# Performance work log

Hardware: AMD Instinct MI355X
Metric: run time of the kernel (lower is better)

## Reference

```python
import jax, jax.numpy as jnp
import numpy as np

PI = 3.14159265359  # TFPI constant from the source


def expected_relu(mu, sigma_sq):
    # Expected ReLU of N(mu, sigma_sq); exact ReLU where sigma_sq == 0 (observed).
    missing = sigma_sq != 0.0
    imputed = jnp.where(missing, sigma_sq, 1e-20)
    s = jnp.sqrt(imputed)
    w = mu / s
    vals = s * (jnp.exp(-0.5 * w * w) / jnp.sqrt(2.0 * PI)
                + 0.5 * w * (1.0 + jax.scipy.special.erf(w / jnp.sqrt(2.0))))
    return jnp.where(missing, vals, 0.5 * (mu + jnp.abs(mu)))


def setup_inputs() -> dict:
    key = jax.random.key(0)
    k0, k1, k2, k3, k4 = jax.random.split(key, 5)
    N, P, C, U = 65536, 256, 3, 512
    x = jax.random.normal(k0, (N, P), dtype=jnp.float32)
    nan_mask = jax.random.bernoulli(k1, 0.15, (N, P))
    x = jnp.where(nan_mask, jnp.nan, x)
    component_means = 0.5 * jax.random.normal(k2, (P, C), dtype=jnp.float32)
    component_vars = jax.random.uniform(k3, (P, C), dtype=jnp.float32, minval=0.5, maxval=1.5)
    component_logits = jnp.ones((C,), dtype=jnp.float32)
    kernel = jax.random.normal(k4, (P, U), dtype=jnp.float32) / np.float32(np.sqrt(P))
    bias = jnp.zeros((U,), dtype=jnp.float32)
    return {"x": x, "component_means": component_means, "component_vars": component_vars,
            "component_logits": component_logits, "kernel": kernel, "bias": bias}


def reference(x, component_means, component_vars, component_logits, kernel, bias):
    # x: [N, P] with NaNs; component_means/vars: [P, C]; logits: [C]; kernel: [P, U]; bias: [U]
    nan_mask = jnp.isnan(x)                       # [N, P]
    x_safe = jnp.where(nan_mask, 0.0, x)          # NaN-free copy (masked out below)
    mu_t = component_means.T                      # [C, P]
    var_t = component_vars.T                      # [C, P]
    # mvn_loglikelihood with NaN entries contributing 0
    q = -jnp.square(x_safe[:, None, :] - mu_t) / var_t / 2.0 - jnp.log(2.0 * PI * var_t) / 2.0  # [N, C, P]
    q = jnp.where(nan_mask[:, None, :], 0.0, q)
    loglik = jnp.sum(q, axis=-1)                  # [N, C]
    reweighted_p = jax.nn.softmax(component_logits + loglik, axis=-1)  # [N, C]
    # Impute missing entries with component means; variance nonzero only where missing
    means = jnp.where(nan_mask[..., None], component_means, x_safe[..., None])   # [N, P, C]
    variances = jnp.where(nan_mask[..., None], component_vars, 0.0)              # [N, P, C]
    layer_mean = jnp.einsum('npc,pu->cnu', means, kernel) + bias                 # [C, N, U]
    layer_var = jnp.einsum('npc,pu->cnu', variances, jnp.square(kernel))         # [C, N, U]
    layer_activation = expected_relu(layer_mean, layer_var)                      # [C, N, U]
    return jnp.einsum('nc,cnu->nu', reweighted_p, layer_activation)              # [N, U]
```

## Files before the change

### kernel.cpp

```cpp
#include <hip/hip_runtime.h>
#include <hip/hip_bf16.h>
#include <math.h>

#define N_ROWS 65536
#define P_DIM  256
#define C_DIM  3
#define U_DIM  512

#define BM 64
#define BU 128
#define NUT (U_DIM / BU)
#define NPL 4
#define NACC 6

typedef __attribute__((ext_vector_type(8))) short short8;
typedef __attribute__((ext_vector_type(4))) float f32x4;
typedef __attribute__((ext_vector_type(4))) float floatx4;
typedef __attribute__((ext_vector_type(4))) unsigned int uint4v;

static __device__ __forceinline__ unsigned short f2bf(float f) {
    unsigned int u = __builtin_bit_cast(unsigned int, f);
    u += 0x7FFFu + ((u >> 16) & 1u);
    return (unsigned short)(u >> 16);
}

static __device__ __forceinline__ float erl(float m, float v) {
    float r = __builtin_amdgcn_rsqf(fmaxf(v, 1e-20f));
    float w = m * r;
    float s = v * r;
    float g = __expf(-0.5f * w * w) * 0.3989422804014327f;
    float aw = fabsf(w);
    float t = __builtin_amdgcn_rcpf(fmaf(0.2316419f, aw, 1.0f));
    float poly = t * (0.319381530f + t * (-0.356563782f + t * (1.781477937f
               + t * (-1.821255978f + t * 1.330274429f))));
    float Phi_pos = 1.0f - g * poly;
    float phi = (w >= 0.0f) ? Phi_pos : 1.0f - Phi_pos;
    float val = s * g + m * phi;
    return (v > 0.0f) ? val : fmaxf(m, 0.0f);
}

__global__ __launch_bounds__(512) void prep_kernel(
    const float* __restrict__ cmeans, const float* __restrict__ cvars,
    const float* __restrict__ kern, unsigned short* __restrict__ Bf,
    float* __restrict__ qtab)
{
    int tid = blockIdx.x * 512 + threadIdx.x;
    const int TOTAL_B = NUT * 8 * 8 * NPL * 64 * 8;
    if (tid < TOTAL_B) {
        int e    = tid & 7;
        int lane = (tid >> 3) & 63;
        int rest = tid >> 9;
        int pl   = rest & 3;
        int ks   = (rest >> 2) & 7;
        int wc   = (rest >> 5) & 7;
        int ut   = rest >> 8;
        int u = ut * BU + wc * 16 + (lane & 15);
        int k = ks * 32 + (lane >> 4) * 8 + e;
        float kv = kern[k * U_DIM + u];
        float val = (pl == 0) ? kv : cvars[k * C_DIM + (pl - 1)] * (kv * kv);
        Bf[tid] = f2bf(val);
    } else if (tid - TOTAL_B < P_DIM) {
        int p = tid - TOTAL_B;
        float a[3], b[3], d[3];
#pragma unroll
        for (int c = 0; c < 3; ++c) {
            float m = cmeans[p * 3 + c];
            float v = cvars[p * 3 + c];
            float iv = 0.5f / v;
            a[c] = iv;
            b[c] = -2.0f * m * iv;
            d[c] = m * m * iv + 0.5f * logf(2.0f * 3.14159265359f * v);
        }
        float* q = qtab + p * 12;
        q[0] = a[0]; q[1] = a[1]; q[2]  = a[2]; q[3]  = 0.f;
        q[4] = b[0]; q[5] = b[1]; q[6]  = b[2]; q[7]  = 0.f;
        q[8] = d[0]; q[9] = d[1]; q[10] = d[2]; q[11] = 0.f;
    }
}

#define LOADB(dst, ksi) do {                                                  \
    _Pragma("unroll")                                                         \
    for (int pl = 0; pl < NPL; ++pl)                                          \
        dst[pl] = *(const short8*)(bpw + ((ksi) * NPL + pl) * 512);           \
} while (0)

#define STEP(breg, ksi) do {                                                  \
    __builtin_amdgcn_s_setprio(1);                                            \
    _Pragma("unroll")                                                         \
    for (int r = 0; r < 2; ++r) {                                             \
        int _ao = aBase + r * 4096 + (ksi) * 512;                             \
        short8 a1 = *(const short8*)&lA1[_ao];                                \
        short8 a2 = *(const short8*)&lA2[_ao];                                \
        short8 a3 = *(const short8*)&lA3[_ao];                                \
        short8 am = *(const short8*)&lMK[_ao];                                \
        acc[0][r] = __builtin_amdgcn_mfma_f32_16x16x32_bf16(a1, breg[0], acc[0][r], 0, 0, 0); \
        acc[1][r] = __builtin_amdgcn_mfma_f32_16x16x32_bf16(a2, breg[0], acc[1][r], 0, 0, 0); \
        acc[2][r] = __builtin_amdgcn_mfma_f32_16x16x32_bf16(a3, breg[0], acc[2][r], 0, 0, 0); \
        acc[3][r] = __builtin_amdgcn_mfma_f32_16x16x32_bf16(am, breg[1], acc[3][r], 0, 0, 0); \
        acc[4][r] = __builtin_amdgcn_mfma_f32_16x16x32_bf16(am, breg[2], acc[4][r], 0, 0, 0); \
        acc[5][r] = __builtin_amdgcn_mfma_f32_16x16x32_bf16(am, breg[3], acc[5][r], 0, 0, 0); \
    }                                                                         \
    __builtin_amdgcn_s_setprio(0);                                            \
} while (0)

__global__ __launch_bounds__(1024, 4) void main_kernel(
    const float* __restrict__ X, const unsigned short* __restrict__ Bf,
    const float* __restrict__ cmeans, const float* __restrict__ qtab,
    const float* __restrict__ logits, const float* __restrict__ bias,
    float* __restrict__ out)
{
    __shared__ unsigned short lA1[BM * P_DIM];
    __shared__ unsigned short lA2[BM * P_DIM];
    __shared__ unsigned short lA3[BM * P_DIM];
    __shared__ unsigned short lMK[BM * P_DIM];
    __shared__ float pws[BM][3];

    const int tid = threadIdx.x;
    const int n0 = blockIdx.x * BM;
    const int lane = tid & 63;
    const int wid  = tid >> 6;
    const int l15  = lane & 15;
    const int lk   = lane >> 4;

    {
        const int rowblk = wid >> 2;
        const float* Xb = X + (size_t)(n0 + rowblk * 16 + l15) * P_DIM + lk * 8;
        const int ebase = rowblk * 4096 + lk * 128 + l15 * 8;
#pragma unroll
        for (int j = 0; j < 2; ++j) {
            int ks = (wid & 3) * 2 + j;
            floatx4 v0 = *(const floatx4*)(Xb + ks * 32);
            floatx4 v1 = *(const floatx4*)(Xb + ks * 32 + 4);
            const float* mup = cmeans + (size_t)(ks * 32 + lk * 8) * 3;
            floatx4 mA = *(const floatx4*)(mup);
            floatx4 mB = *(const floatx4*)(mup + 4);
            floatx4 mC = *(const floatx4*)(mup + 8);
            floatx4 mD = *(const floatx4*)(mup + 12);
            floatx4 mE = *(const floatx4*)(mup + 16);
            floatx4 mF = *(const floatx4*)(mup + 20);
            float mu[24];
#pragma unroll
            for (int z = 0; z < 4; ++z) {
                mu[z] = mA[z]; mu[4 + z] = mB[z]; mu[8 + z] = mC[z];
                mu[12 + z] = mD[z]; mu[16 + z] = mE[z]; mu[20 + z] = mF[z];
            }
            unsigned int w1[4], w2[4], w3[4], wm[4];
#pragma unroll
            for (int pe = 0; pe < 4; ++pe) {
#pragma unroll
                for (int h = 0; h < 2; ++h) {
                    int e = pe * 2 + h;
                    float x = (e < 4) ? v0[e] : v1[e - 4];
                    bool na = !(x == x);
                    unsigned int b1 = (unsigned int)f2bf(na ? mu[e * 3 + 0] : x);
                    unsigned int b2 = (unsigned int)f2bf(na ? mu[e * 3 + 1] : x);
                    unsigned int b3 = (unsigned int)f2bf(na ? mu[e * 3 + 2] : x);
                    unsigned int bm = na ? 0x3F80u : 0u;
                    if (h == 0) { w1[pe] = b1; w2[pe] = b2; w3[pe] = b3; wm[pe] = bm; }
                    else { w1[pe] |= b1 << 16; w2[pe] |= b2 << 16; w3[pe] |= b3 << 16; wm[pe] |= bm << 16; }
                }
            }
            int idx = ebase + ks * 512;
            *(uint4v*)&lA1[idx] = (uint4v){w1[0], w1[1], w1[2], w1[3]};
            *(uint4v*)&lA2[idx] = (uint4v){w2[0], w2[1], w2[2], w2[3]};
            *(uint4v*)&lA3[idx] = (uint4v){w3[0], w3[1], w3[2], w3[3]};
            *(uint4v*)&lMK[idx] = (uint4v){wm[0], wm[1], wm[2], wm[3]};
        }
    }

    {
        int row = tid >> 4;
        int sub = tid & 15;
        const floatx4* xr = (const floatx4*)(X + (size_t)(n0 + row) * P_DIM);
        const floatx4* qt = (const floatx4*)qtab;
        float a0 = 0.f, a1 = 0.f, a2 = 0.f;
#pragma unroll
        for (int i = 0; i < 4; ++i) {
            floatx4 v = xr[sub * 4 + i];
#pragma unroll
            for (int e = 0; e < 4; ++e) {
                float x = v[e];
                int p = sub * 16 + i * 4 + e;
                bool valid = (x == x);
                float xv = valid ? x : 0.f;
                floatx4 qa = qt[p * 3 + 0];
                floatx4 qb = qt[p * 3 + 1];
                floatx4 qd = qt[p * 3 + 2];
                float q0 = fmaf(fmaf(qa[0], xv, qb[0]), xv, qd[0]);
                float q1 = fmaf(fmaf(qa[1], xv, qb[1]), xv, qd[1]);
                float q2 = fmaf(fmaf(qa[2], xv, qb[2]), xv, qd[2]);
                a0 += valid ? q0 : 0.f;
                a1 += valid ? q1 : 0.f;
                a2 += valid ? q2 : 0.f;
            }
        }
#pragma unroll
        for (int off = 1; off < 16; off <<= 1) {
            a0 += __shfl_xor(a0, off);
            a1 += __shfl_xor(a1, off);
            a2 += __shfl_xor(a2, off);
        }
        if (sub == 0) {
            float z0 = logits[0] - a0;
            float z1 = logits[1] - a1;
            float z2 = logits[2] - a2;
            float mx = fmaxf(z0, fmaxf(z1, z2));
            float e0 = __expf(z0 - mx), e1 = __expf(z1 - mx), e2 = __expf(z2 - mx);
            float inv = __builtin_amdgcn_rcpf(e0 + e1 + e2);
            pws[row][0] = e0 * inv;
            pws[row][1] = e1 * inv;
            pws[row][2] = e2 * inv;
        }
    }
    __syncthreads();

    const int wr   = wid >> 3;
    const int wc   = wid & 7;
    const int aBase = wr * 8192 + lk * 128 + l15 * 8;
    const int phase = wc & 3;

#pragma unroll 1
    for (int ut0 = 0; ut0 < NUT; ++ut0) {
        const int ut = (ut0 + phase) & (NUT - 1);
        const unsigned short* bpw = Bf + ((size_t)(ut * 8 + wc) * (8 * NPL * 512)) + (size_t)lane * 8;

        f32x4 acc[NACC][2];
#pragma unroll
        for (int pl = 0; pl < NACC; ++pl)
#pragma unroll
            for (int r = 0; r < 2; ++r)
                acc[pl][r] = (f32x4){0.f, 0.f, 0.f, 0.f};

        short8 bA[NPL], bB[NPL];
        LOADB(bA, 0);
#pragma unroll 1
        for (int ks = 0; ks < 8; ks += 2) {
            LOADB(bB, ks + 1);
            STEP(bA, ks);
            if (ks + 2 < 8) LOADB(bA, ks + 2);
            STEP(bB, ks + 1);
        }

        const int ucol = ut * BU + wc * 16 + l15;
        const float bias_u = bias[ucol];
#pragma unroll
        for (int r = 0; r < 2; ++r) {
            int rloc = wr * 32 + r * 16 + 4 * lk;
#pragma unroll
            for (int q = 0; q < 4; ++q) {
                int rl = rloc + q;
                float p0 = pws[rl][0], p1 = pws[rl][1], p2 = pws[rl][2];
                float res = p0 * erl(acc[0][r][q] + bias_u, acc[3][r][q])
                          + p1 * erl(acc[1][r][q] + bias_u, acc[4][r][q])
                          + p2 * erl(acc[2][r][q] + bias_u, acc[5][r][q]);
                out[(size_t)(n0 + rl) * U_DIM + ucol] = res;
            }
        }
    }
}

extern "C" void kernel_launch(void* const* d_in, const int* in_sizes, int n_in,
                              void* d_out, int out_size, void* d_ws, size_t ws_size,
                              hipStream_t stream)
{
    const float* X      = (const float*)d_in[0];
    const float* cmeans = (const float*)d_in[1];
    const float* cvars  = (const float*)d_in[2];
    const float* logits = (const float*)d_in[3];
    const float* kern   = (const float*)d_in[4];
    const float* bias   = (const float*)d_in[5];
    float* out = (float*)d_out;

    char* wsb = (char*)d_ws;
    unsigned short* Bf = (unsigned short*)wsb;
    float* qtab = (float*)(wsb + 1048576);

    hipLaunchKernelGGL(prep_kernel, dim3(1025), dim3(512), 0, stream,
                       cmeans, cvars, kern, Bf, qtab);
    hipLaunchKernelGGL(main_kernel, dim3(N_ROWS / BM), dim3(1024), 0, stream,
                       X, Bf, cmeans, qtab, logits, bias, out);
}
```

Measured before the change: 276.9 us.

## Halve row tile to 32 with 512-thread blocks and row-major A staging

Shrinks the per-block row tile from 64 to 32 rows and the block size from 1024 to 512 threads, so each of the 8 waves now covers a single 32-row strip and one 16-column slice. The A-staging phase is rewritten so each thread converts 16 contiguous elements of one X row and loads only the component means it needs, instead of preloading 24 means. Smaller blocks use less LDS and should let more blocks fit per CU, improving occupancy and load balance. The cost is that B tiles are reloaded from global memory twice as often per row of output.

```diff
diff --git a/kernel.cpp b/kernel.cpp
--- a/kernel.cpp
+++ b/kernel.cpp
@@ -7,7 +7,7 @@
 #define C_DIM  3
 #define U_DIM  512
 
-#define BM 64
+#define BM 32
 #define BU 128
 #define NUT (U_DIM / BU)
 #define NPL 4
@@ -103,7 +103,7 @@
     __builtin_amdgcn_s_setprio(0);                                            \
 } while (0)
 
-__global__ __launch_bounds__(1024, 4) void main_kernel(
+__global__ __launch_bounds__(512, 4) void main_kernel(
     const float* __restrict__ X, const unsigned short* __restrict__ Bf,
     const float* __restrict__ cmeans, const float* __restrict__ qtab,
     const float* __restrict__ logits, const float* __restrict__ bias,
@@ -123,44 +123,39 @@
     const int lk   = lane >> 4;
 
     {
-        const int rowblk = wid >> 2;
-        const float* Xb = X + (size_t)(n0 + rowblk * 16 + l15) * P_DIM + lk * 8;
-        const int ebase = rowblk * 4096 + lk * 128 + l15 * 8;
-#pragma unroll
-        for (int j = 0; j < 2; ++j) {
-            int ks = (wid & 3) * 2 + j;
-            floatx4 v0 = *(const floatx4*)(Xb + ks * 32);
-            floatx4 v1 = *(const floatx4*)(Xb + ks * 32 + 4);
-            const float* mup = cmeans + (size_t)(ks * 32 + lk * 8) * 3;
-            floatx4 mA = *(const floatx4*)(mup);
-            floatx4 mB = *(const floatx4*)(mup + 4);
-            floatx4 mC = *(const floatx4*)(mup + 8);
-            floatx4 mD = *(const floatx4*)(mup + 12);
-            floatx4 mE = *(const floatx4*)(mup + 16);
-            floatx4 mF = *(const floatx4*)(mup + 20);
-            float mu[24];
-#pragma unroll
-            for (int z = 0; z < 4; ++z) {
-                mu[z] = mA[z]; mu[4 + z] = mB[z]; mu[8 + z] = mC[z];
-                mu[12 + z] = mD[z]; mu[16 + z] = mE[z]; mu[20 + z] = mF[z];
-            }
+        const int row = tid >> 4;
+        const int sub = tid & 15;
+        const float* Xr = X + (size_t)(n0 + row) * P_DIM;
+#pragma unroll
+        for (int h = 0; h < 2; ++h) {
+            int k0 = sub * 16 + h * 8;
+            floatx4 v0 = *(const floatx4*)(Xr + k0);
+            floatx4 v1 = *(const floatx4*)(Xr + k0 + 4);
+            const float* mup = cmeans + (size_t)k0 * 3;
             unsigned int w1[4], w2[4], w3[4], wm[4];
 #pragma unroll
             for (int pe = 0; pe < 4; ++pe) {
-#pragma unroll
-                for (int h = 0; h < 2; ++h) {
-                    int e = pe * 2 + h;
+                floatx4 mlo = *(const floatx4*)(mup + pe * 6);
+                floatx4 mhi = *(const floatx4*)(mup + pe * 6 + 4);
+#pragma unroll
+                for (int hh = 0; hh < 2; ++hh) {
+                    int e = pe * 2 + hh;
                     float x = (e < 4) ? v0[e] : v1[e - 4];
                     bool na = !(x == x);
-                    unsigned int b1 = (unsigned int)f2bf(na ? mu[e * 3 + 0] : x);
-                    unsigned int b2 = (unsigned int)f2bf(na ? mu[e * 3 + 1] : x);
-                    unsigned int b3 = (unsigned int)f2bf(na ? mu[e * 3 + 2] : x);
+                    float m1 = (hh == 0) ? mlo[0] : mlo[3];
+                    float m2 = (hh == 0) ? mlo[1] : mhi[0];
+                    float m3 = (hh == 0) ? mlo[2] : mhi[1];
+                    unsigned int b1 = (unsigned int)f2bf(na ? m1 : x);
+                    unsigned int b2 = (unsigned int)f2bf(na ? m2 : x);
+                    unsigned int b3 = (unsigned int)f2bf(na ? m3 : x);
                     unsigned int bm = na ? 0x3F80u : 0u;
-                    if (h == 0) { w1[pe] = b1; w2[pe] = b2; w3[pe] = b3; wm[pe] = bm; }
+                    if (hh == 0) { w1[pe] = b1; w2[pe] = b2; w3[pe] = b3; wm[pe] = bm; }
                     else { w1[pe] |= b1 << 16; w2[pe] |= b2 << 16; w3[pe] |= b3 << 16; wm[pe] |= bm << 16; }
                 }
             }
-            int idx = ebase + ks * 512;
+            int ks = k0 >> 5;
+            int lkk = (k0 >> 3) & 3;
+            int idx = (row >> 4) * 4096 + ks * 512 + lkk * 128 + (row & 15) * 8;
             *(uint4v*)&lA1[idx] = (uint4v){w1[0], w1[1], w1[2], w1[3]};
             *(uint4v*)&lA2[idx] = (uint4v){w2[0], w2[1], w2[2], w2[3]};
             *(uint4v*)&lA3[idx] = (uint4v){w3[0], w3[1], w3[2], w3[3]};
@@ -214,9 +209,8 @@
     }
     __syncthreads();
 
-    const int wr   = wid >> 3;
-    const int wc   = wid & 7;
-    const int aBase = wr * 8192 + lk * 128 + l15 * 8;
+    const int wc = wid;
+    const int aBase = lk * 128 + l15 * 8;
     const int phase = wc & 3;
 
 #pragma unroll 1
@@ -245,7 +239,7 @@
         const float bias_u = bias[ucol];
 #pragma unroll
         for (int r = 0; r < 2; ++r) {
-            int rloc = wr * 32 + r * 16 + 4 * lk;
+            int rloc = r * 16 + 4 * lk;
 #pragma unroll
             for (int q = 0; q < 4; ++q) {
                 int rl = rloc + q;
@@ -277,6 +271,6 @@
 
     hipLaunchKernelGGL(prep_kernel, dim3(1025), dim3(512), 0, stream,
                        cmeans, cvars, kern, Bf, qtab);
-    hipLaunchKernelGGL(main_kernel, dim3(N_ROWS / BM), dim3(1024), 0, stream,
+    hipLaunchKernelGGL(main_kernel, dim3(N_ROWS / BM), dim3(512), 0, stream,
                        X, Bf, cmeans, qtab, logits, bias, out);
 }
```

Measured after the change: 264.7 us. 4.4% less time.
